# Performance work log

Measured on AMD Instinct MI355X. Metric: run time of the kernel, lower is better.

## Reference

```python
import jax, jax.numpy as jnp
import numpy as np

TEMP = 5.0  # temperature_init
# All C(4,2)=6 keep-2-of-4 patterns for 2:4 semi-structured sparsity
PATTERNS = jnp.array([[1,1,0,0],[1,0,1,0],[1,0,0,1],[0,1,1,0],[0,1,0,1],[0,0,1,1]], dtype=jnp.float32)


def masked_linear(x, w, b, alpha, ids):
    # x: [N, I], w: [O, I], alpha: [A, O, I//4, 6], ids: [N]
    A, O, G, P = alpha.shape
    probs = jax.nn.softmax(alpha / TEMP, axis=-1)            # [A, O, G, 6]
    mask = jnp.einsum('aogp,pk->aogk', probs, PATTERNS)      # [A, O, G, 4]
    wm = w[None, :, :] * mask.reshape(A, O, G * 4)           # [A, O, I] per-agent masked weight
    y = jnp.einsum('ni,aoi->nao', x, wm)                     # dense per-agent GEMM
    y = jnp.take_along_axis(y, ids[:, None, None], axis=1)[:, 0, :]
    return y + b


def gru_cell(x, h, w_ih, w_hh, b_ih, b_hh):
    gi = x @ w_ih.T + b_ih
    gh = h @ w_hh.T + b_hh
    i_r, i_z, i_n = jnp.split(gi, 3, axis=-1)
    h_r, h_z, h_n = jnp.split(gh, 3, axis=-1)
    r = jax.nn.sigmoid(i_r + h_r)
    z = jax.nn.sigmoid(i_z + h_z)
    n = jnp.tanh(i_n + r * h_n)
    return (1.0 - z) * n + z * h


def setup_inputs() -> dict:
    key = jax.random.key(0)
    ks = jax.random.split(key, 20)
    B, A, E, H, NA = 1024, 8, 64, 512, 16
    s = 0.05
    d = {}
    d['inputs'] = jax.random.normal(ks[0], (B, A, E), jnp.float32)
    d['hidden_state'] = jax.random.normal(ks[1], (B, A, H), jnp.float32)
    d['agent_ids'] = jax.random.randint(ks[2], (B, A), 0, A, jnp.int32)
    d['fc1_w'] = jax.random.normal(ks[3], (H, E), jnp.float32) * s
    d['fc1_b'] = jax.random.normal(ks[4], (H,), jnp.float32) * s
    d['fc1_alpha'] = jax.random.normal(ks[5], (A, H, E // 4, 6), jnp.float32)
    d['gru_w_ih'] = jax.random.normal(ks[6], (3 * H, H), jnp.float32) * s
    d['gru_w_hh'] = jax.random.normal(ks[7], (3 * H, H), jnp.float32) * s
    d['gru_b_ih'] = jax.random.normal(ks[8], (3 * H,), jnp.float32) * s
    d['gru_b_hh'] = jax.random.normal(ks[9], (3 * H,), jnp.float32) * s
    d['fc2_w'] = jax.random.normal(ks[10], (H, H), jnp.float32) * s
    d['fc2_b'] = jax.random.normal(ks[11], (H,), jnp.float32) * s
    d['fc2_alpha'] = jax.random.normal(ks[12], (A, H, H // 4, 6), jnp.float32)
    d['fc3_w'] = jax.random.normal(ks[13], (H, H), jnp.float32) * s
    d['fc3_b'] = jax.random.normal(ks[14], (H,), jnp.float32) * s
    d['fc3_alpha'] = jax.random.normal(ks[15], (A, H, H // 4, 6), jnp.float32)
    d['fc4_w'] = jax.random.normal(ks[16], (NA, H), jnp.float32) * s
    d['fc4_b'] = jax.random.normal(ks[17], (NA,), jnp.float32) * s
    d['fc4_alpha'] = jax.random.normal(ks[18], (A, NA, H // 4, 6), jnp.float32)
    return d


def reference(inputs, hidden_state, agent_ids,
              fc1_w, fc1_b, fc1_alpha,
              gru_w_ih, gru_w_hh, gru_b_ih, gru_b_hh,
              fc2_w, fc2_b, fc2_alpha,
              fc3_w, fc3_b, fc3_alpha,
              fc4_w, fc4_b, fc4_alpha):
    b, a, e = inputs.shape
    H = hidden_state.shape[-1]
    x = inputs.reshape(-1, e)
    ids = agent_ids.reshape(-1)
    x = jax.nn.relu(masked_linear(x, fc1_w, fc1_b, fc1_alpha, ids))
    h = gru_cell(x, hidden_state.reshape(-1, H), gru_w_ih, gru_w_hh, gru_b_ih, gru_b_hh)
    q = jax.nn.relu(masked_linear(h, fc2_w, fc2_b, fc2_alpha, ids))
    q = jax.nn.relu(masked_linear(q, fc3_w, fc3_b, fc3_alpha, ids))
    q = masked_linear(q, fc4_w, fc4_b, fc4_alpha, ids)
    return q.reshape(b, a, -1), h.reshape(b, a, -1)
```

## Files before the change

kernel.cpp:

```cpp
#include <hip/hip_runtime.h>
#include <hip/hip_bf16.h>

typedef unsigned short ushort_t;
typedef __bf16 bf16x8 __attribute__((ext_vector_type(8)));
typedef unsigned short us8 __attribute__((ext_vector_type(8)));
typedef float f32x4 __attribute__((ext_vector_type(4)));

__device__ __forceinline__ float b2f(ushort_t h) {
    union { unsigned int u; float f; } v; v.u = ((unsigned int)h) << 16; return v.f;
}
__device__ __forceinline__ ushort_t f2b(float f) {
    union { float f; unsigned int u; } v; v.f = f;
    unsigned int u = v.u;
    unsigned int r = (u + 0x7FFFu + ((u >> 16) & 1u)) >> 16;
    return (ushort_t)r;
}
__device__ __forceinline__ float sigmoidf_(float x) {
    return 1.f / (1.f + __expf(-x));
}
__device__ __forceinline__ void store_o(ushort_t* p, float v) { *p = f2b(v); }
__device__ __forceinline__ void store_o(float* p, float v) { *p = v; }

__global__ void fill_kernel(float* out, long long n, float val) {
    long long i = (long long)blockIdx.x * blockDim.x + threadIdx.x;
    if (i < n) out[i] = val;
}

#define PACKSZ(O, K) ((long long)((O) >= 64 ? (O) >> 6 : 1) * ((K) >> 5) * 2048)

__global__ void sort_kernel(const int* __restrict__ ids, int N,
                            int* __restrict__ perm, int* __restrict__ seg,
                            int4* __restrict__ ttab, int* __restrict__ tcount) {
    __shared__ int hist[16][8];
    __shared__ int wbase[16][8];
    __shared__ int atot[8];
    __shared__ int abase[8];
    int tid = threadIdx.x, wave = tid >> 6, lane = tid & 63;
    int base = wave * 512;
    unsigned long long lt = (lane == 63) ? 0x7fffffffffffffffull
                                         : ((1ull << lane) - 1ull);
    int myid[8], rank[8];
    int run[8] = {0, 0, 0, 0, 0, 0, 0, 0};
    #pragma unroll
    for (int i = 0; i < 8; i++) myid[i] = ids[base + i * 64 + lane] & 7;
    #pragma unroll
    for (int i = 0; i < 8; i++) {
        int a = myid[i];
        int r = 0;
        #pragma unroll
        for (int a2 = 0; a2 < 8; a2++) {
            unsigned long long m = __ballot(a == a2);
            if (a2 == a) r = run[a2] + __popcll(m & lt);
            run[a2] += __popcll(m);
        }
        rank[i] = r;
    }
    if (lane == 0) {
        #pragma unroll
        for (int a = 0; a < 8; a++) hist[wave][a] = run[a];
    }
    __syncthreads();
    if (tid < 8) {
        int a = tid, s = 0;
        for (int w = 0; w < 16; w++) { wbase[w][a] = s; s += hist[w][a]; }
        atot[a] = s;
    }
    __syncthreads();
    if (tid == 0) {
        int s = 0;
        for (int a = 0; a < 8; a++) { abase[a] = s; seg[a] = s; s += atot[a]; }
        seg[8] = s;
        int T = 0;
        for (int a = 0; a < 8; a++)
            for (int m = abase[a]; m < abase[a] + atot[a]; m += 64) {
                int e = abase[a] + atot[a];
                if (e > m + 64) e = m + 64;
                ttab[T++] = make_int4(a, m, e, 0);
            }
        *tcount = T;
    }
    __syncthreads();
    #pragma unroll
    for (int i = 0; i < 8; i++) {
        int a = myid[i];
        perm[abase[a] + wbase[wave][a] + rank[i]] = base + i * 64 + lane;
    }
}

__device__ __forceinline__ void maskw_item(const float* __restrict__ alpha,
                                           const float* __restrict__ w,
                                           ushort_t* __restrict__ wm,
                                           long long idx, int O, int G, int dup) {
    int g = (int)(idx % G);
    long long t2 = idx / G;
    int o = (int)(t2 % O);
    int a = (int)(t2 / O);
    const float* al = alpha + idx * 6;
    float p[6];
    float mx = -1e30f;
    #pragma unroll
    for (int i = 0; i < 6; i++) { p[i] = al[i] * 0.2f; mx = fmaxf(mx, p[i]); }
    float s = 0.f;
    #pragma unroll
    for (int i = 0; i < 6; i++) { p[i] = __expf(p[i] - mx); s += p[i]; }
    float inv = 1.f / s;
    #pragma unroll
    for (int i = 0; i < 6; i++) p[i] *= inv;
    float mk[4] = { p[0] + p[1] + p[2], p[0] + p[3] + p[4],
                    p[1] + p[3] + p[5], p[2] + p[4] + p[5] };
    int K = G * 4;
    const float* wr = w + (long long)o * K + g * 4;
    ushort_t* base = wm + (long long)a * PACKSZ(O, K);
    int k0 = g * 4;
    int c = o >> 6, su = (o >> 4) & 3, n = o & 15;
    int kk = k0 >> 5, q = (k0 >> 3) & 3, e0 = k0 & 7;
    long long off = (((long long)(c * (K >> 5) + kk) * 4 + su) * 64 + (q * 16 + n)) * 8 + e0;
    #pragma unroll
    for (int t = 0; t < 4; t++) {
        ushort_t v = f2b(wr[t] * mk[t]);
        base[off + t] = v;
        if (dup) {
            base[off + t + 512] = v;
            base[off + t + 1024] = v;
            base[off + t + 1536] = v;
        }
    }
}

__device__ __forceinline__ void canon_gather_item(const float* __restrict__ src,
                                                  ushort_t* __restrict__ dst,
                                                  const int* __restrict__ perm,
                                                  int ld, long long i) {
    long long base = i * 8;
    int pos = (int)(base / ld);
    int k = (int)(base % ld);
    int row = perm[pos] & 8191;
    const float* s = src + (long long)row * ld + k;
    us8 v;
    #pragma unroll
    for (int e = 0; e < 8; e++) v[e] = f2b(s[e]);
    *(us8*)(dst + base) = v;
}

__device__ __forceinline__ void canon_pack_item(const float* __restrict__ src,
                                                ushort_t* __restrict__ dst,
                                                long long i) {
    long long base = i * 8;
    int o_full = (int)(base >> 9);
    int k0 = (int)(base & 511);
    int g = o_full >> 9, o = o_full & 511;
    int c = o >> 6, su = (o >> 4) & 3, n = o & 15;
    int kk = k0 >> 5, q = (k0 >> 3) & 3;
    long long off = (long long)g * 262144 +
        (((long long)(c * 16 + kk) * 4 + su) * 64 + (q * 16 + n)) * 8;
    us8 v;
    #pragma unroll
    for (int e = 0; e < 8; e++) v[e] = f2b(src[base + e]);
    *(us8*)(dst + off) = v;
}

#define PB0 256
#define PB1 2048
#define PB2 2048
#define PB3 64
#define PB4 256
#define PB5 2048
#define PB6 384
#define PB7 384
#define PREP_BLOCKS (PB0+PB1+PB2+PB3+PB4+PB5+PB6+PB7)

__global__ void prep_kernel(const float* fc1_al, const float* fc1_w, ushort_t* wm1,
                            const float* fc2_al, const float* fc2_w, ushort_t* wm2,
                            const float* fc3_al, const float* fc3_w, ushort_t* wm3,
                            const float* fc4_al, const float* fc4_w, ushort_t* wm4,
                            const float* inputs, ushort_t* inp_pos,
                            const float* hidden, ushort_t* hid_pos,
                            const float* wih, ushort_t* wihp,
                            const float* whh, ushort_t* whhp,
                            const int* perm) {
    int b = blockIdx.x;
    int tid = threadIdx.x;
    if (b < PB0) { maskw_item(fc1_al, fc1_w, wm1, (long long)b * 256 + tid, 512, 16, 0); return; }
    b -= PB0;
    if (b < PB1) { maskw_item(fc2_al, fc2_w, wm2, (long long)b * 256 + tid, 512, 128, 0); return; }
    b -= PB1;
    if (b < PB2) { maskw_item(fc3_al, fc3_w, wm3, (long long)b * 256 + tid, 512, 128, 0); return; }
    b -= PB2;
    if (b < PB3) { maskw_item(fc4_al, fc4_w, wm4, (long long)b * 256 + tid, 16, 128, 1); return; }
    b -= PB3;
    if (b < PB4) { canon_gather_item(inputs, inp_pos, perm, 64, (long long)b * 256 + tid); return; }
    b -= PB4;
    if (b < PB5) { canon_gather_item(hidden, hid_pos, perm, 512, (long long)b * 256 + tid); return; }
    b -= PB5;
    if (b < PB6) { canon_pack_item(wih, wihp, (long long)b * 256 + tid); return; }
    b -= PB6;
    canon_pack_item(whh, whhp, (long long)b * 256 + tid);
}

#define BM 64
#define BN 64

template <typename OT>
__launch_bounds__(256, 4)
__global__ void gemm_tiled(const ushort_t* __restrict__ In, int ldin,
                           const ushort_t* __restrict__ Wpk, long long wstride,
                           const float* __restrict__ bias,
                           OT* __restrict__ Out, int ldo,
                           const int4* __restrict__ ttab,
                           const int* __restrict__ tcount,
                           const int* __restrict__ scatter,
                           int O, int K, int relu) {
    int t = blockIdx.x;
    if (t >= *tcount) return;
    int4 tt = ttab[t];
    int a = tt.x, pos0 = tt.y, pos1 = tt.z;
    int o0 = blockIdx.y * BN;

    __shared__ ushort_t As[2048];

    int tid = threadIdx.x;
    int wave = tid >> 6, lane = tid & 63;
    int wr = (wave >> 1) & 1, wc = wave & 1;
    int quad = lane >> 4, l16 = lane & 15;
    int srow = tid >> 2, sgrp = tid & 3;
    int wsoff = (srow * 4 + (sgrp ^ ((srow >> 2) & 3))) * 8;
    int rl = (l16 * 4 + (quad ^ ((l16 >> 2) & 3))) * 8;

    int apos = pos0 + srow;
    int apos_c = apos < pos1 ? apos : (pos1 - 1);
    const ushort_t* aptr = In + (long long)apos_c * ldin + sgrp * 8;

    const ushort_t* wb = Wpk + (long long)a * wstride +
        (long long)blockIdx.y * (K >> 5) * 2048 + lane * 8;

    f32x4 acc[2][2];
    #pragma unroll
    for (int i = 0; i < 2; i++)
        #pragma unroll
        for (int j = 0; j < 2; j++) acc[i][j] = (f32x4){0.f, 0.f, 0.f, 0.f};

    int KK = K >> 5;
    us8 av = *(const us8*)(aptr);
    bf16x8 vb0 = *(const bf16x8*)(wb + (wc * 2 + 0) * 512);
    bf16x8 vb1 = *(const bf16x8*)(wb + (wc * 2 + 1) * 512);
    us8 avn = av;
    bf16x8 nb0 = vb0, nb1 = vb1;

    for (int kk = 0; kk < KK; kk++) {
        __syncthreads();
        *(us8*)(&As[wsoff]) = av;
        if (kk + 1 < KK) {
            avn = *(const us8*)(aptr + (kk + 1) * 32);
            nb0 = *(const bf16x8*)(wb + ((kk + 1) * 4 + wc * 2 + 0) * 512);
            nb1 = *(const bf16x8*)(wb + ((kk + 1) * 4 + wc * 2 + 1) * 512);
        }
        __syncthreads();
        bf16x8 af[2];
        af[0] = *(const bf16x8*)(&As[(wr * 2 + 0) * 512 + rl]);
        af[1] = *(const bf16x8*)(&As[(wr * 2 + 1) * 512 + rl]);
        #pragma unroll
        for (int i = 0; i < 2; i++) {
            acc[i][0] = __builtin_amdgcn_mfma_f32_16x16x32_bf16(af[i], vb0, acc[i][0], 0, 0, 0);
            acc[i][1] = __builtin_amdgcn_mfma_f32_16x16x32_bf16(af[i], vb1, acc[i][1], 0, 0, 0);
        }
        av = avn; vb0 = nb0; vb1 = nb1;
    }

    #pragma unroll
    for (int i = 0; i < 2; i++) {
        int mbase = wr * 32 + i * 16 + quad * 4;
        #pragma unroll
        for (int j = 0; j < 2; j++) {
            int col = o0 + wc * 32 + j * 16 + l16;
            if (col < O) {
                float bias_v = bias ? bias[col] : 0.f;
                #pragma unroll
                for (int r = 0; r < 4; r++) {
                    int pos = pos0 + mbase + r;
                    if (pos < pos1) {
                        float v = acc[i][j][r] + bias_v;
                        if (relu) v = fmaxf(v, 0.f);
                        int orow = (scatter ? scatter[pos] : pos) & 8191;
                        store_o(&Out[(long long)orow * ldo + col], v);
                    }
                }
            }
        }
    }
}

__launch_bounds__(256, 3)
__global__ void gru_fused(const ushort_t* __restrict__ y1,
                          const ushort_t* __restrict__ hid_pos,
                          const float* __restrict__ hidden_f,
                          const ushort_t* __restrict__ wihp,
                          const ushort_t* __restrict__ whhp,
                          const float* __restrict__ bih,
                          const float* __restrict__ bhh,
                          const int* __restrict__ perm,
                          float* __restrict__ out_h_f,
                          ushort_t* __restrict__ hp,
                          int N, int H) {
    int m0 = blockIdx.x * 64;

    __shared__ ushort_t Ay[2048];
    __shared__ ushort_t Ah[2048];
    __shared__ ushort_t Bt[6][2048];

    int tid = threadIdx.x;
    int wave = tid >> 6, lane = tid & 63;
    int wr = (wave >> 1) & 1, wc = wave & 1;
    int quad = lane >> 4, l16 = lane & 15;
    int srow = tid >> 2, sgrp = tid & 3;
    int wsoff = (srow * 4 + (sgrp ^ ((srow >> 2) & 3))) * 8;
    int rl = (l16 * 4 + (quad ^ ((l16 >> 2) & 3))) * 8;

    const ushort_t* ay_p = y1 + (long long)(m0 + srow) * H + sgrp * 8;
    const ushort_t* ah_p = hid_pos + (long long)(m0 + srow) * H + sgrp * 8;

    long long cb = (long long)blockIdx.y * 16 * 2048 + tid * 8;
    const ushort_t* wbg[6];
    #pragma unroll
    for (int g = 0; g < 3; g++) wbg[g] = wihp + (long long)g * 262144 + cb;
    #pragma unroll
    for (int g = 3; g < 6; g++) wbg[g] = whhp + (long long)(g - 3) * 262144 + cb;

    f32x4 acc[4][2][2];
    #pragma unroll
    for (int g = 0; g < 4; g++)
        #pragma unroll
        for (int i = 0; i < 2; i++)
            #pragma unroll
            for (int j = 0; j < 2; j++) acc[g][i][j] = (f32x4){0.f, 0.f, 0.f, 0.f};

    us8 va = *(const us8*)(ay_p);
    us8 vh = *(const us8*)(ah_p);
    us8 vb[6];
    #pragma unroll
    for (int g = 0; g < 6; g++) vb[g] = *(const us8*)(wbg[g]);

    for (int kk = 0; kk < 16; kk++) {
        __syncthreads();
        *(us8*)(&Ay[wsoff]) = va;
        *(us8*)(&Ah[wsoff]) = vh;
        #pragma unroll
        for (int g = 0; g < 6; g++) *(us8*)(&Bt[g][tid * 8]) = vb[g];
        if (kk < 15) {
            va = *(const us8*)(ay_p + (kk + 1) * 32);
            vh = *(const us8*)(ah_p + (kk + 1) * 32);
            #pragma unroll
            for (int g = 0; g < 6; g++) vb[g] = *(const us8*)(wbg[g] + (kk + 1) * 2048);
        }
        __syncthreads();

        bf16x8 ayf[2], ahf[2];
        #pragma unroll
        for (int u = 0; u < 2; u++) {
            ayf[u] = *(const bf16x8*)(&Ay[(wr * 2 + u) * 512 + rl]);
            ahf[u] = *(const bf16x8*)(&Ah[(wr * 2 + u) * 512 + rl]);
        }
        #pragma unroll
        for (int g = 0; g < 3; g++) {
            bf16x8 bw[2], bu[2];
            #pragma unroll
            for (int u = 0; u < 2; u++) {
                bw[u] = *(const bf16x8*)(&Bt[g][(wc * 2 + u) * 512 + lane * 8]);
                bu[u] = *(const bf16x8*)(&Bt[g + 3][(wc * 2 + u) * 512 + lane * 8]);
            }
            int ai = (g < 2) ? g : 2;
            int ah2 = (g < 2) ? g : 3;
            #pragma unroll
            for (int i = 0; i < 2; i++)
                #pragma unroll
                for (int j = 0; j < 2; j++) {
                    acc[ai][i][j] = __builtin_amdgcn_mfma_f32_16x16x32_bf16(
                        ayf[i], bw[j], acc[ai][i][j], 0, 0, 0);
                    acc[ah2][i][j] = __builtin_amdgcn_mfma_f32_16x16x32_bf16(
                        ahf[i], bu[j], acc[ah2][i][j], 0, 0, 0);
                }
        }
    }

    int c0 = blockIdx.y * 64;
    #pragma unroll
    for (int i = 0; i < 2; i++) {
        #pragma unroll
        for (int r = 0; r < 4; r++) {
            int pos = m0 + wr * 32 + i * 16 + quad * 4 + r;
            int norig = perm[pos] & 8191;
            #pragma unroll
            for (int j = 0; j < 2; j++) {
                int col = c0 + wc * 32 + j * 16 + l16;
                float sr = acc[0][i][j][r] + bih[col] + bhh[col];
                float sz = acc[1][i][j][r] + bih[H + col] + bhh[H + col];
                float in_ = acc[2][i][j][r] + bih[2 * H + col];
                float hn = acc[3][i][j][r] + bhh[2 * H + col];
                float rg = sigmoidf_(sr);
                float zg = sigmoidf_(sz);
                float ng = tanhf(in_ + rg * hn);
                float hv = hidden_f[(long long)norig * H + col];
                float hnew = (1.f - zg) * ng + zg * hv;
                out_h_f[(long long)norig * H + col] = hnew;
                hp[(long long)pos * H + col] = f2b(hnew);
            }
        }
    }
}

extern "C" void kernel_launch(void* const* d_in, const int* in_sizes, int n_in,
                              void* d_out, int out_size, void* d_ws, size_t ws_size,
                              hipStream_t stream) {
    (void)in_sizes; (void)n_in;
    const int N = 8192, A = 8, E = 64, H = 512, NA = 16;

    float* out_f = (float*)d_out;
    float* out_q = out_f;
    float* out_h = out_f + (size_t)N * NA;

    char* p = (char*)d_ws;
    auto alloc = [&](size_t b) { char* r = p; p += (b + 255) & ~(size_t)255; return r; };
    int*  perm   = (int*)alloc((size_t)N * 4);
    int*  seg    = (int*)alloc(16 * 4);
    int4* ttab   = (int4*)alloc(144 * 16);
    int*  tcount = (int*)alloc(256);
    ushort_t* wm1     = (ushort_t*)alloc((size_t)A * PACKSZ(H, E) * 2);
    ushort_t* wm2     = (ushort_t*)alloc((size_t)A * PACKSZ(H, H) * 2);
    ushort_t* wm3     = (ushort_t*)alloc((size_t)A * PACKSZ(H, H) * 2);
    ushort_t* wm4     = (ushort_t*)alloc((size_t)A * PACKSZ(NA, H) * 2);
    ushort_t* y1      = (ushort_t*)alloc((size_t)N * H * 2);
    ushort_t* inp_pos = (ushort_t*)alloc((size_t)N * E * 2);
    ushort_t* hid_pos = (ushort_t*)alloc((size_t)N * H * 2);
    ushort_t* wihp    = (ushort_t*)alloc((size_t)3 * H * H * 2);
    ushort_t* whhp    = (ushort_t*)alloc((size_t)3 * H * H * 2);
    ushort_t* hp      = (ushort_t*)alloc((size_t)N * H * 2);
    size_t need = (size_t)(p - (char*)d_ws);
    ushort_t* q2 = y1;
    ushort_t* q3 = hid_pos;

    if (ws_size < need) {
        fill_kernel<<<(unsigned)((out_size + 255) / 256), 256, 0, stream>>>(
            out_f, out_size, 1000.f);
        return;
    }

    const float* inputs = (const float*)d_in[0];
    const float* hidden = (const float*)d_in[1];
    const int*   ids    = (const int*)d_in[2];
    const float* fc1_w  = (const float*)d_in[3];
    const float* fc1_b  = (const float*)d_in[4];
    const float* fc1_al = (const float*)d_in[5];
    const float* wih    = (const float*)d_in[6];
    const float* whh    = (const float*)d_in[7];
    const float* bih    = (const float*)d_in[8];
    const float* bhh    = (const float*)d_in[9];
    const float* fc2_w  = (const float*)d_in[10];
    const float* fc2_b  = (const float*)d_in[11];
    const float* fc2_al = (const float*)d_in[12];
    const float* fc3_w  = (const float*)d_in[13];
    const float* fc3_b  = (const float*)d_in[14];
    const float* fc3_al = (const float*)d_in[15];
    const float* fc4_w  = (const float*)d_in[16];
    const float* fc4_b  = (const float*)d_in[17];
    const float* fc4_al = (const float*)d_in[18];

    sort_kernel<<<1, 1024, 0, stream>>>(ids, N, perm, seg, ttab, tcount);

    prep_kernel<<<PREP_BLOCKS, 256, 0, stream>>>(
        fc1_al, fc1_w, wm1, fc2_al, fc2_w, wm2, fc3_al, fc3_w, wm3,
        fc4_al, fc4_w, wm4, inputs, inp_pos, hidden, hid_pos,
        wih, wihp, whh, whhp, perm);

    dim3 blk(256);
    gemm_tiled<ushort_t><<<dim3(136, H / BN), blk, 0, stream>>>(
        inp_pos, E, wm1, PACKSZ(H, E), fc1_b, y1, H, ttab, tcount,
        nullptr, H, E, 1);
    gru_fused<<<dim3(N / 64, H / 64), blk, 0, stream>>>(
        y1, hid_pos, hidden, wihp, whhp, bih, bhh, perm, out_h, hp, N, H);
    gemm_tiled<ushort_t><<<dim3(136, H / BN), blk, 0, stream>>>(
        hp, H, wm2, PACKSZ(H, H), fc2_b, q2, H, ttab, tcount,
        nullptr, H, H, 1);
    gemm_tiled<ushort_t><<<dim3(136, H / BN), blk, 0, stream>>>(
        q2, H, wm3, PACKSZ(H, H), fc3_b, q3, H, ttab, tcount,
        nullptr, H, H, 1);
    gemm_tiled<float><<<dim3(136, 1), blk, 0, stream>>>(
        q3, H, wm4, PACKSZ(NA, H), fc4_b, out_q, NA, ttab, tcount,
        perm, NA, H, 0);
}
```

Baseline: 231.3 us.

## Widen masked GEMM tiles to 128 columns and restructure barriers with prefetch-before-store

The masked per-agent GEMMs now use a templated tile width: fc1-fc3 use 128 output columns per block, with each wave covering 64 columns, so each A tile in shared memory feeds twice as many MFMAs and half as many blocks are launched. Both the GEMM and the GRU kernel replace __syncthreads with raw s_barrier helpers plus sched_barrier. Next-iteration global loads are issued before the shared-memory store, and only lgkmcnt is waited on before the second barrier, to overlap global latency. The GRU kernel adds double-buffered register staging for this. The cost is more registers per thread, which may lower occupancy, and fewer blocks for the GEMMs.

```diff
diff --git a/kernel.cpp b/kernel.cpp
--- a/kernel.cpp
+++ b/kernel.cpp
@@ -20,6 +20,19 @@
 }
 __device__ __forceinline__ void store_o(ushort_t* p, float v) { *p = f2b(v); }
 __device__ __forceinline__ void store_o(float* p, float v) { *p = v; }
+
+__device__ __forceinline__ void bar_raw() {
+    asm volatile("" ::: "memory");
+    __builtin_amdgcn_s_barrier();
+    asm volatile("" ::: "memory");
+    __builtin_amdgcn_sched_barrier(0);
+}
+__device__ __forceinline__ void bar_lgkm() {
+    asm volatile("s_waitcnt lgkmcnt(0)" ::: "memory");
+    __builtin_amdgcn_s_barrier();
+    asm volatile("" ::: "memory");
+    __builtin_amdgcn_sched_barrier(0);
+}
 
 __global__ void fill_kernel(float* out, long long n, float val) {
     long long i = (long long)blockIdx.x * blockDim.x + threadIdx.x;
@@ -197,10 +210,7 @@
     canon_pack_item(whh, whhp, (long long)b * 256 + tid);
 }
 
-#define BM 64
-#define BN 64
-
-template <typename OT>
+template <typename OT, int NC>
 __launch_bounds__(256, 4)
 __global__ void gemm_tiled(const ushort_t* __restrict__ In, int ldin,
                            const ushort_t* __restrict__ Wpk, long long wstride,
@@ -214,7 +224,8 @@
     if (t >= *tcount) return;
     int4 tt = ttab[t];
     int a = tt.x, pos0 = tt.y, pos1 = tt.z;
-    int o0 = blockIdx.y * BN;
+    int o0 = blockIdx.y * (64 * NC);
+    constexpr int JJ = 2 * NC;
 
     __shared__ ushort_t As[2048];
 
@@ -230,48 +241,59 @@
     int apos_c = apos < pos1 ? apos : (pos1 - 1);
     const ushort_t* aptr = In + (long long)apos_c * ldin + sgrp * 8;
 
+    int c_idx = blockIdx.y * NC + (NC == 2 ? wc : 0);
     const ushort_t* wb = Wpk + (long long)a * wstride +
-        (long long)blockIdx.y * (K >> 5) * 2048 + lane * 8;
-
-    f32x4 acc[2][2];
+        (long long)c_idx * (K >> 5) * 2048 + lane * 8;
+
+    f32x4 acc[2][JJ];
     #pragma unroll
     for (int i = 0; i < 2; i++)
         #pragma unroll
-        for (int j = 0; j < 2; j++) acc[i][j] = (f32x4){0.f, 0.f, 0.f, 0.f};
+        for (int j = 0; j < JJ; j++) acc[i][j] = (f32x4){0.f, 0.f, 0.f, 0.f};
 
     int KK = K >> 5;
     us8 av = *(const us8*)(aptr);
-    bf16x8 vb0 = *(const bf16x8*)(wb + (wc * 2 + 0) * 512);
-    bf16x8 vb1 = *(const bf16x8*)(wb + (wc * 2 + 1) * 512);
+    bf16x8 vb[JJ], nb[JJ];
+    #pragma unroll
+    for (int j = 0; j < JJ; j++) {
+        int su = (NC == 2) ? j : wc * 2 + j;
+        vb[j] = *(const bf16x8*)(wb + su * 512);
+        nb[j] = vb[j];
+    }
     us8 avn = av;
-    bf16x8 nb0 = vb0, nb1 = vb1;
 
     for (int kk = 0; kk < KK; kk++) {
-        __syncthreads();
-        *(us8*)(&As[wsoff]) = av;
+        bar_raw();
         if (kk + 1 < KK) {
             avn = *(const us8*)(aptr + (kk + 1) * 32);
-            nb0 = *(const bf16x8*)(wb + ((kk + 1) * 4 + wc * 2 + 0) * 512);
-            nb1 = *(const bf16x8*)(wb + ((kk + 1) * 4 + wc * 2 + 1) * 512);
-        }
-        __syncthreads();
+            #pragma unroll
+            for (int j = 0; j < JJ; j++) {
+                int su = (NC == 2) ? j : wc * 2 + j;
+                nb[j] = *(const bf16x8*)(wb + ((kk + 1) * 4 + su) * 512);
+            }
+        }
+        *(us8*)(&As[wsoff]) = av;
+        bar_lgkm();
         bf16x8 af[2];
         af[0] = *(const bf16x8*)(&As[(wr * 2 + 0) * 512 + rl]);
         af[1] = *(const bf16x8*)(&As[(wr * 2 + 1) * 512 + rl]);
         #pragma unroll
-        for (int i = 0; i < 2; i++) {
-            acc[i][0] = __builtin_amdgcn_mfma_f32_16x16x32_bf16(af[i], vb0, acc[i][0], 0, 0, 0);
-            acc[i][1] = __builtin_amdgcn_mfma_f32_16x16x32_bf16(af[i], vb1, acc[i][1], 0, 0, 0);
-        }
-        av = avn; vb0 = nb0; vb1 = nb1;
+        for (int i = 0; i < 2; i++)
+            #pragma unroll
+            for (int j = 0; j < JJ; j++)
+                acc[i][j] = __builtin_amdgcn_mfma_f32_16x16x32_bf16(af[i], vb[j], acc[i][j], 0, 0, 0);
+        av = avn;
+        #pragma unroll
+        for (int j = 0; j < JJ; j++) vb[j] = nb[j];
     }
 
     #pragma unroll
     for (int i = 0; i < 2; i++) {
         int mbase = wr * 32 + i * 16 + quad * 4;
         #pragma unroll
-        for (int j = 0; j < 2; j++) {
-            int col = o0 + wc * 32 + j * 16 + l16;
+        for (int j = 0; j < JJ; j++) {
+            int su = (NC == 2) ? j : wc * 2 + j;
+            int col = o0 + (NC == 2 ? wc * 64 : 0) + su * 16 + l16;
             if (col < O) {
                 float bias_v = bias ? bias[col] : 0.f;
                 #pragma unroll
@@ -335,23 +357,24 @@
 
     us8 va = *(const us8*)(ay_p);
     us8 vh = *(const us8*)(ah_p);
-    us8 vb[6];
-    #pragma unroll
-    for (int g = 0; g < 6; g++) vb[g] = *(const us8*)(wbg[g]);
+    us8 vb[6], vb2[6];
+    #pragma unroll
+    for (int g = 0; g < 6; g++) { vb[g] = *(const us8*)(wbg[g]); vb2[g] = vb[g]; }
+    us8 va2 = va, vh2 = vh;
 
     for (int kk = 0; kk < 16; kk++) {
-        __syncthreads();
+        bar_raw();
+        if (kk < 15) {
+            va2 = *(const us8*)(ay_p + (kk + 1) * 32);
+            vh2 = *(const us8*)(ah_p + (kk + 1) * 32);
+            #pragma unroll
+            for (int g = 0; g < 6; g++) vb2[g] = *(const us8*)(wbg[g] + (kk + 1) * 2048);
+        }
         *(us8*)(&Ay[wsoff]) = va;
         *(us8*)(&Ah[wsoff]) = vh;
         #pragma unroll
         for (int g = 0; g < 6; g++) *(us8*)(&Bt[g][tid * 8]) = vb[g];
-        if (kk < 15) {
-            va = *(const us8*)(ay_p + (kk + 1) * 32);
-            vh = *(const us8*)(ah_p + (kk + 1) * 32);
-            #pragma unroll
-            for (int g = 0; g < 6; g++) vb[g] = *(const us8*)(wbg[g] + (kk + 1) * 2048);
-        }
-        __syncthreads();
+        bar_lgkm();
 
         bf16x8 ayf[2], ahf[2];
         #pragma unroll
@@ -379,6 +402,9 @@
                         ahf[i], bu[j], acc[ah2][i][j], 0, 0, 0);
                 }
         }
+        va = va2; vh = vh2;
+        #pragma unroll
+        for (int g = 0; g < 6; g++) vb[g] = vb2[g];
     }
 
     int c0 = blockIdx.y * 64;
@@ -471,18 +497,18 @@
         wih, wihp, whh, whhp, perm);
 
     dim3 blk(256);
-    gemm_tiled<ushort_t><<<dim3(136, H / BN), blk, 0, stream>>>(
+    gemm_tiled<ushort_t, 2><<<dim3(136, H / 128), blk, 0, stream>>>(
         inp_pos, E, wm1, PACKSZ(H, E), fc1_b, y1, H, ttab, tcount,
         nullptr, H, E, 1);
     gru_fused<<<dim3(N / 64, H / 64), blk, 0, stream>>>(
         y1, hid_pos, hidden, wihp, whhp, bih, bhh, perm, out_h, hp, N, H);
-    gemm_tiled<ushort_t><<<dim3(136, H / BN), blk, 0, stream>>>(
+    gemm_tiled<ushort_t, 2><<<dim3(136, H / 128), blk, 0, stream>>>(
         hp, H, wm2, PACKSZ(H, H), fc2_b, q2, H, ttab, tcount,
         nullptr, H, H, 1);
-    gemm_tiled<ushort_t><<<dim3(136, H / BN), blk, 0, stream>>>(
+    gemm_tiled<ushort_t, 2><<<dim3(136, H / 128), blk, 0, stream>>>(
         q2, H, wm3, PACKSZ(H, H), fc3_b, q3, H, ttab, tcount,
         nullptr, H, H, 1);
-    gemm_tiled<float><<<dim3(136, 1), blk, 0, stream>>>(
+    gemm_tiled<float, 1><<<dim3(136, 1), blk, 0, stream>>>(
         q3, H, wm4, PACKSZ(NA, H), fc4_b, out_q, NA, ttab, tcount,
         perm, NA, H, 0);
 }
```

Measured after the change: 237.3 us. 1.03x slower.
